# Performance work log

Measured on AMD Instinct MI355X. Metric: run time of the kernel, lower is better.

The kernel has to match this reference:

```python
import jax, jax.numpy as jnp
import numpy as np
import math

B, S, D, H = 2, 2048, 1024, 16
HD = D // H  # head_dims = 64


def setup_inputs() -> dict:
    key = jax.random.key(0)
    ks = jax.random.split(key, 8)
    sc = 1.0 / math.sqrt(D)
    return {
        "queries": jax.random.normal(ks[0], (B, S, D), jnp.float32),
        "keys":    jax.random.normal(ks[1], (B, S, D), jnp.float32),
        "values":  jax.random.normal(ks[2], (B, S, D), jnp.float32),
        # causal mask: 1 where attending allowed, 0 where blocked (masked_fill on ==0)
        "mask": jnp.tril(jnp.ones((S, S), jnp.int32)),
        "Wq": jax.random.normal(ks[3], (D, D), jnp.float32) * sc,
        "bq": jnp.zeros((D,), jnp.float32),
        "Wk": jax.random.normal(ks[4], (D, D), jnp.float32) * sc,
        "bk": jnp.zeros((D,), jnp.float32),
        "Wv": jax.random.normal(ks[5], (D, D), jnp.float32) * sc,
        "bv": jnp.zeros((D,), jnp.float32),
        "Wo": jax.random.normal(ks[6], (D, D), jnp.float32) * sc,
        "bo": jnp.zeros((D,), jnp.float32),
    }


def _split_heads(x):
    # (B, S, D) -> (B, H, S, HD)
    return x.reshape(B, S, H, HD).transpose(0, 2, 1, 3)


def reference(queries, keys, values, mask, Wq, bq, Wk, bk, Wv, bv, Wo, bo):
    q = queries @ Wq + bq
    k = keys @ Wk + bk
    # NOTE: faithful to source quirk — V is projected from the ALREADY-PROJECTED keys
    # (original: keys = self.W_keys(keys); values = self.W_values(keys))
    v = k @ Wv + bv
    q, k, v = _split_heads(q), _split_heads(k), _split_heads(v)
    # naive full NxN attention, as in the source
    scores = jnp.einsum("bhqd,bhkd->bhqk", q, k) / math.sqrt(HD)
    scores = jnp.where(mask == 0, jnp.float32(-1e9), scores)
    probs = jax.nn.softmax(scores, axis=-1)
    attn = jnp.einsum("bhqk,bhkd->bhqd", probs, v)
    attn = attn.transpose(0, 2, 1, 3).reshape(B, S, D)
    return attn @ Wo + bo
```

## Files before the change

kernel.cpp:

```cpp
#include <hip/hip_runtime.h>

typedef unsigned short u16;
typedef unsigned int u32;
typedef __bf16 bf16x8 __attribute__((ext_vector_type(8)));
typedef float f32x4 __attribute__((ext_vector_type(4)));

#define MFMA16(a, b, c) __builtin_amdgcn_mfma_f32_16x16x32_bf16(a, b, c, 0, 0, 0)

__device__ __forceinline__ void gload16(const void* g, void* l) {
  __builtin_amdgcn_global_load_lds((const __attribute__((address_space(1))) void*)g,
                                   (__attribute__((address_space(3))) void*)l, 16, 0, 0);
}

__device__ __forceinline__ u16 f2bf(float f) {
  u32 u = __builtin_bit_cast(u32, f);
  u += 0x7fffu + ((u >> 16) & 1u);
  return (u16)(u >> 16);
}
__device__ __forceinline__ u32 pack2(float a, float b) {
  return (u32)f2bf(a) | ((u32)f2bf(b) << 16);
}

__global__ __launch_bounds__(256) void cvt_kernel(const float* __restrict__ q,
                                                  const float* __restrict__ k,
                                                  u16* __restrict__ qb,
                                                  u16* __restrict__ kb) {
  const float* src = blockIdx.y ? k : q;
  u16* dst = blockIdx.y ? kb : qb;
  size_t i = (size_t)blockIdx.x * 256 + threadIdx.x;
  float4 v = ((const float4*)src)[i];
  ushort4 o;
  o.x = f2bf(v.x); o.y = f2bf(v.y); o.z = f2bf(v.z); o.w = f2bf(v.w);
  ((ushort4*)dst)[i] = o;
}

__global__ __launch_bounds__(256) void wtrans_kernel(const float* W0, const float* W1,
                                                     const float* W2, const float* W3,
                                                     u16* T0, u16* T1, u16* T2, u16* T3) {
  int z = blockIdx.z;
  const float* W = z == 0 ? W0 : z == 1 ? W1 : z == 2 ? W2 : W3;
  u16* T = z == 0 ? T0 : z == 1 ? T1 : z == 2 ? T2 : T3;
  __shared__ float tile[64][65];
  int tr = blockIdx.y * 64, tc = blockIdx.x * 64;
  int tid = threadIdx.x;
  int c4 = (tid & 15) * 4, r0 = tid >> 4;
#pragma unroll
  for (int i = 0; i < 4; i++) {
    int r = r0 + i * 16;
    float4 v = *(const float4*)(W + (size_t)(tr + r) * 1024 + tc + c4);
    tile[r][c4 + 0] = v.x; tile[r][c4 + 1] = v.y;
    tile[r][c4 + 2] = v.z; tile[r][c4 + 3] = v.w;
  }
  __syncthreads();
#pragma unroll
  for (int i = 0; i < 2; i++) {
    int c = tid + i * 256;
    int n = c >> 3, kg = c & 7;
    uint4 o;
    o.x = pack2(tile[kg * 8 + 0][n], tile[kg * 8 + 1][n]);
    o.y = pack2(tile[kg * 8 + 2][n], tile[kg * 8 + 3][n]);
    o.z = pack2(tile[kg * 8 + 4][n], tile[kg * 8 + 5][n]);
    o.w = pack2(tile[kg * 8 + 6][n], tile[kg * 8 + 7][n]);
    *(uint4*)(T + (size_t)(tc + n) * 1024 + tr + kg * 8) = o;
  }
}

template <int MODE>
__global__ __launch_bounds__(256) void gemm_kernel(
    const u16* A0, const u16* B0, const float* bias0, void* C0, float scale0,
    const u16* A1, const u16* B1, const float* bias1, void* C1, float scale1,
    int M, int N, int K) {
  const u16* A = A0; const u16* Bt = B0; const float* bias = bias0; void* Cout = C0;
  float scale = scale0;
  if (blockIdx.z) { A = A1; Bt = B1; bias = bias1; Cout = C1; scale = scale1; }

  __shared__ __attribute__((aligned(16))) char sAB[49152];
  const int tid = threadIdx.x, lane = tid & 63, w = tid >> 6;
  const int l15 = lane & 15, quad = lane >> 4;
  const int wm = (w >> 1) * 64, wn = (w & 1) * 32;
  const int m0 = blockIdx.y * 128, n0 = blockIdx.x * 64;

  const int lrow = lane >> 3, lcg = (lane & 7) ^ lrow;
  const u16* aP[4]; const u16* bP[2];
#pragma unroll
  for (int i = 0; i < 4; i++)
    aP[i] = A + (size_t)(m0 + w * 32 + i * 8 + lrow) * K + lcg * 8;
#pragma unroll
  for (int i = 0; i < 2; i++)
    bP[i] = Bt + (size_t)(n0 + w * 16 + i * 8 + lrow) * K + lcg * 8;

  int aoff[4], boff[2];
#pragma unroll
  for (int t = 0; t < 4; t++) {
    int ra = wm + t * 16 + l15;
    aoff[t] = ra * 128 + ((quad ^ (ra & 7)) * 16);
  }
#pragma unroll
  for (int t = 0; t < 2; t++) {
    int rb = wn + t * 16 + l15;
    boff[t] = 16384 + rb * 128 + ((quad ^ (rb & 7)) * 16);
  }

#pragma unroll
  for (int i = 0; i < 4; i++) { gload16(aP[i], sAB + w * 4096 + i * 1024); aP[i] += 64; }
#pragma unroll
  for (int i = 0; i < 2; i++) { gload16(bP[i], sAB + 16384 + w * 2048 + i * 1024); bP[i] += 64; }

  f32x4 acc[4][2] = {};
  int cur = 0;
  for (int k = 0; k < K; k += 64) {
    __syncthreads();
    if (k + 64 < K) {
      char* dst = sAB + (cur ^ 1) * 24576;
#pragma unroll
      for (int i = 0; i < 4; i++) { gload16(aP[i], dst + w * 4096 + i * 1024); aP[i] += 64; }
#pragma unroll
      for (int i = 0; i < 2; i++) { gload16(bP[i], dst + 16384 + w * 2048 + i * 1024); bP[i] += 64; }
    }
    const char* buf = sAB + cur * 24576;
#pragma unroll
    for (int kt = 0; kt < 2; kt++) {
      bf16x8 af[4], bfr[2];
#pragma unroll
      for (int t = 0; t < 4; t++) af[t] = *(const bf16x8*)(buf + (aoff[t] ^ (kt * 64)));
#pragma unroll
      for (int t = 0; t < 2; t++) bfr[t] = *(const bf16x8*)(buf + (boff[t] ^ (kt * 64)));
#pragma unroll
      for (int mt = 0; mt < 4; mt++)
#pragma unroll
        for (int nt = 0; nt < 2; nt++)
          acc[mt][nt] = MFMA16(af[mt], bfr[nt], acc[mt][nt]);
    }
    cur ^= 1;
  }

#pragma unroll
  for (int nt = 0; nt < 2; nt++) {
    int col = n0 + wn + nt * 16 + l15;
    float bv = bias[col];
#pragma unroll
    for (int mt = 0; mt < 4; mt++) {
      int row = m0 + wm + mt * 16 + quad * 4;
      if (MODE == 0) {
        u16* C = (u16*)Cout;
#pragma unroll
        for (int r = 0; r < 4; r++)
          C[(size_t)(row + r) * N + col] = f2bf((acc[mt][nt][r] + bv) * scale);
      } else if (MODE == 1) {
        u16* C = (u16*)Cout;
        int hh = col >> 6, hd = col & 63;
        int bb = row >> 11, s = row & 2047;
        ushort4 o;
        o.x = f2bf((acc[mt][nt][0] + bv) * scale);
        o.y = f2bf((acc[mt][nt][1] + bv) * scale);
        o.z = f2bf((acc[mt][nt][2] + bv) * scale);
        o.w = f2bf((acc[mt][nt][3] + bv) * scale);
        *(ushort4*)(C + ((size_t)((bb * 16 + hh) * 64 + hd) * 2048 + s)) = o;
      } else {
        float* C = (float*)Cout;
#pragma unroll
        for (int r = 0; r < 4; r++)
          C[(size_t)(row + r) * N + col] = (acc[mt][nt][r] + bv) * scale;
      }
    }
  }
}

__global__ __launch_bounds__(256) void attn_kernel(const u16* __restrict__ qw,
                                                   const u16* __restrict__ kw,
                                                   const u16* __restrict__ vw,
                                                   u16* __restrict__ aout) {
  __shared__ __attribute__((aligned(16))) char sQ[8192];
  __shared__ __attribute__((aligned(16))) char sKV[2][16384];
  __shared__ __attribute__((aligned(16))) char sP[8192];
  const int bh = blockIdx.x, p = blockIdx.y;
  const int b = bh >> 4, h = bh & 15;
  const int tid = threadIdx.x, lane = tid & 63, w = tid >> 6;
  const int l15 = lane & 15, quad = lane >> 4;
  const int lrow = lane >> 3, lcg = (lane & 7) ^ lrow;
  const u16* kb0 = kw + (size_t)(b * 2048) * 1024 + h * 64;
  const u16* vb0 = vw + (size_t)bh * 64 * 2048;

  int qoff[2], poff[2], koff[2][4], voff[2][4], wroff[4];
#pragma unroll
  for (int kt = 0; kt < 2; kt++) {
    int qrow = w * 16 + l15;
    qoff[kt] = qrow * 128 + (((kt * 4 + quad) ^ (qrow & 7)) * 16);
    poff[kt] = w * 2048 + l15 * 128 + (((kt * 4 + quad) ^ (l15 & 7)) * 16);
#pragma unroll
    for (int mt = 0; mt < 4; mt++) {
      int r2 = mt * 16 + l15;
      koff[kt][mt] = r2 * 128 + (((kt * 4 + quad) ^ (r2 & 7)) * 16);
      voff[kt][mt] = 8192 + koff[kt][mt];
    }
  }
#pragma unroll
  for (int mt = 0; mt < 4; mt++)
    wroff[mt] = w * 2048 + l15 * 128 + (((2 * mt + (quad >> 1)) ^ (l15 & 7)) * 16) +
                (quad & 1) * 8;

  for (int phase = 0; phase < 2; ++phase) {
    const int t = phase ? (31 - p) : p;
    __syncthreads();
    {
      const u16* qbase = qw + (size_t)(b * 2048 + t * 64) * 1024 + h * 64;
#pragma unroll
      for (int i = 0; i < 2; i++) {
        int r = w * 16 + i * 8 + lrow;
        gload16(qbase + (size_t)r * 1024 + lcg * 8, sQ + w * 2048 + i * 1024);
        gload16(kb0 + (size_t)r * 1024 + lcg * 8, sKV[0] + w * 2048 + i * 1024);
        gload16(vb0 + (size_t)r * 2048 + lcg * 8, sKV[0] + 8192 + w * 2048 + i * 1024);
      }
    }

    float ls[4] = {0.f, 0.f, 0.f, 0.f};
    f32x4 o[4] = {};
    for (int j = 0; j < t; ++j) {
      __syncthreads();
      {
        char* dstb = sKV[(j + 1) & 1];
#pragma unroll
        for (int i = 0; i < 2; i++) {
          int r = w * 16 + i * 8 + lrow;
          gload16(kb0 + (size_t)((j + 1) * 64 + r) * 1024 + lcg * 8,
                  dstb + w * 2048 + i * 1024);
          gload16(vb0 + (size_t)r * 2048 + (j + 1) * 64 + lcg * 8,
                  dstb + 8192 + w * 2048 + i * 1024);
        }
      }
      const char* bufb = sKV[j & 1];

      f32x4 st[4] = {};
#pragma unroll
      for (int kt = 0; kt < 2; ++kt) {
        bf16x8 qf = *(const bf16x8*)(sQ + qoff[kt]);
        bf16x8 kf[4];
#pragma unroll
        for (int mt = 0; mt < 4; mt++) kf[mt] = *(const bf16x8*)(bufb + koff[kt][mt]);
#pragma unroll
        for (int mt = 0; mt < 4; mt++) st[mt] = MFMA16(kf[mt], qf, st[mt]);
      }
#pragma unroll
      for (int mt = 0; mt < 4; mt++) {
        float e0 = __builtin_amdgcn_exp2f(st[mt][0]);
        float e1 = __builtin_amdgcn_exp2f(st[mt][1]);
        float e2 = __builtin_amdgcn_exp2f(st[mt][2]);
        float e3 = __builtin_amdgcn_exp2f(st[mt][3]);
        ls[mt] += (e0 + e1) + (e2 + e3);
        *(uint2*)(sP + wroff[mt]) = make_uint2(pack2(e0, e1), pack2(e2, e3));
      }
      __asm__ volatile("" ::: "memory");
#pragma unroll
      for (int kt = 0; kt < 2; ++kt) {
        bf16x8 pf = *(const bf16x8*)(sP + poff[kt]);
        bf16x8 vf[4];
#pragma unroll
        for (int mt = 0; mt < 4; mt++) vf[mt] = *(const bf16x8*)(bufb + voff[kt][mt]);
#pragma unroll
        for (int mt = 0; mt < 4; mt++) o[mt] = MFMA16(vf[mt], pf, o[mt]);
      }
    }

    {
      __syncthreads();
      const char* bufb = sKV[t & 1];
      f32x4 st[4] = {};
#pragma unroll
      for (int kt = 0; kt < 2; ++kt) {
        bf16x8 qf = *(const bf16x8*)(sQ + qoff[kt]);
        bf16x8 kf[4];
#pragma unroll
        for (int mt = 0; mt < 4; mt++) kf[mt] = *(const bf16x8*)(bufb + koff[kt][mt]);
#pragma unroll
        for (int mt = 0; mt < 4; mt++) st[mt] = MFMA16(kf[mt], qf, st[mt]);
      }
      const int qcol = w * 16 + l15;
#pragma unroll
      for (int mt = 0; mt < 4; mt++) {
        float e[4];
#pragma unroll
        for (int r = 0; r < 4; r++) {
          float ev = __builtin_amdgcn_exp2f(st[mt][r]);
          if (mt * 16 + quad * 4 + r > qcol) ev = 0.f;
          e[r] = ev;
        }
        ls[mt] += (e[0] + e[1]) + (e[2] + e[3]);
        *(uint2*)(sP + wroff[mt]) = make_uint2(pack2(e[0], e[1]), pack2(e[2], e[3]));
      }
      __asm__ volatile("" ::: "memory");
#pragma unroll
      for (int kt = 0; kt < 2; ++kt) {
        bf16x8 pf = *(const bf16x8*)(sP + poff[kt]);
        bf16x8 vf[4];
#pragma unroll
        for (int mt = 0; mt < 4; mt++) vf[mt] = *(const bf16x8*)(bufb + voff[kt][mt]);
#pragma unroll
        for (int mt = 0; mt < 4; mt++) o[mt] = MFMA16(vf[mt], pf, o[mt]);
      }
    }

    float lsum = (ls[0] + ls[1]) + (ls[2] + ls[3]);
    lsum += __shfl_xor(lsum, 16, 64);
    lsum += __shfl_xor(lsum, 32, 64);
    float inv = 1.0f / lsum;
    int token = b * 2048 + t * 64 + w * 16 + l15;
#pragma unroll
    for (int mt = 0; mt < 4; mt++) {
      int d0 = h * 64 + mt * 16 + quad * 4;
      ushort4 ov;
      ov.x = f2bf(o[mt][0] * inv);
      ov.y = f2bf(o[mt][1] * inv);
      ov.z = f2bf(o[mt][2] * inv);
      ov.w = f2bf(o[mt][3] * inv);
      *(ushort4*)(aout + (size_t)token * 1024 + d0) = ov;
    }
  }
}

extern "C" void kernel_launch(void* const* d_in, const int* in_sizes, int n_in,
                              void* d_out, int out_size, void* d_ws, size_t ws_size,
                              hipStream_t stream) {
  const float* queries = (const float*)d_in[0];
  const float* keys    = (const float*)d_in[1];
  const float* Wq = (const float*)d_in[4];
  const float* bq = (const float*)d_in[5];
  const float* Wk = (const float*)d_in[6];
  const float* bk = (const float*)d_in[7];
  const float* Wv = (const float*)d_in[8];
  const float* bv = (const float*)d_in[9];
  const float* Wo = (const float*)d_in[10];
  const float* bo = (const float*)d_in[11];

  char* ws = (char*)d_ws;
  u16* qb  = (u16*)(ws);
  u16* kb  = (u16*)(ws + (8u << 20));
  u16* qP  = (u16*)(ws + (16u << 20));
  u16* kP  = (u16*)(ws);
  u16* vP  = (u16*)(ws + (8u << 20));
  u16* WqT = (u16*)(ws + (24u << 20));
  u16* WkT = (u16*)(ws + (26u << 20));
  u16* WvT = (u16*)(ws + (28u << 20));
  u16* WoT = (u16*)(ws + (30u << 20));

  const float kscale = 1.4426950408889634f / 8.0f;

  cvt_kernel<<<dim3(4096, 2), 256, 0, stream>>>(queries, keys, qb, kb);
  wtrans_kernel<<<dim3(16, 16, 4), 256, 0, stream>>>(Wq, Wk, Wv, Wo, WqT, WkT, WvT, WoT);
  gemm_kernel<0><<<dim3(16, 32, 2), 256, 0, stream>>>(
      qb, WqT, bq, qP, kscale, kb, WkT, bk, kP, 1.0f, 4096, 1024, 1024);
  gemm_kernel<1><<<dim3(16, 32, 1), 256, 0, stream>>>(
      kP, WvT, bv, vP, 1.0f, kP, WvT, bv, vP, 1.0f, 4096, 1024, 1024);
  attn_kernel<<<dim3(32, 16), 256, 0, stream>>>(qP, kP, vP, qP);
  gemm_kernel<2><<<dim3(16, 32, 1), 256, 0, stream>>>(
      qP, WoT, bo, d_out, 1.0f, qP, WoT, bo, d_out, 1.0f, 4096, 1024, 1024);
}
```

Before: 221.4 us.

## Restructure attention kernel with 32x32 MFMA, split-KV waves, and register-resident P

Rewrites the attention kernel to use 32x32x16 bf16 MFMA tiles. Each pair of waves covers 32 query columns, and the two waves in a pair process alternate KV tiles (split-K) out of a 4-slot LDS ring. Q fragments are held in registers, and P is passed from the QK^T output to the PV input through permlane32_swap instead of an LDS round-trip. Partial outputs are merged across the wave pair through shared memory at the end. The aim is fewer LDS accesses and syncs per tile and better MFMA efficiency. The costs are higher register pressure (launch bounds 256,2), 64KB of LDS, and an extra reduction step.

```diff
diff --git a/kernel.cpp b/kernel.cpp
--- a/kernel.cpp
+++ b/kernel.cpp
@@ -4,8 +4,11 @@
 typedef unsigned int u32;
 typedef __bf16 bf16x8 __attribute__((ext_vector_type(8)));
 typedef float f32x4 __attribute__((ext_vector_type(4)));
+typedef float f32x16 __attribute__((ext_vector_type(16)));
+typedef unsigned int u32x4v __attribute__((ext_vector_type(4)));
 
 #define MFMA16(a, b, c) __builtin_amdgcn_mfma_f32_16x16x32_bf16(a, b, c, 0, 0, 0)
+#define MFMA32(a, b, c) __builtin_amdgcn_mfma_f32_32x32x16_bf16(a, b, c, 0, 0, 0)
 
 __device__ __forceinline__ void gload16(const void* g, void* l) {
   __builtin_amdgcn_global_load_lds((const __attribute__((address_space(1))) void*)g,
@@ -166,153 +169,154 @@
   }
 }
 
-__global__ __launch_bounds__(256) void attn_kernel(const u16* __restrict__ qw,
-                                                   const u16* __restrict__ kw,
-                                                   const u16* __restrict__ vw,
-                                                   u16* __restrict__ aout) {
-  __shared__ __attribute__((aligned(16))) char sQ[8192];
-  __shared__ __attribute__((aligned(16))) char sKV[2][16384];
-  __shared__ __attribute__((aligned(16))) char sP[8192];
+__global__ __launch_bounds__(256, 2) void attn_kernel(const u16* __restrict__ qw,
+                                                      const u16* __restrict__ kw,
+                                                      const u16* __restrict__ vw,
+                                                      u16* __restrict__ aout) {
+  __shared__ __attribute__((aligned(16))) char sKV[4][16384];
   const int bh = blockIdx.x, p = blockIdx.y;
   const int b = bh >> 4, h = bh & 15;
   const int tid = threadIdx.x, lane = tid & 63, w = tid >> 6;
-  const int l15 = lane & 15, quad = lane >> 4;
+  const int g = w & 1, qh = w >> 1;
+  const int c = lane & 31, hi = lane >> 5;
+  const int qcol = qh * 32 + c;
   const int lrow = lane >> 3, lcg = (lane & 7) ^ lrow;
   const u16* kb0 = kw + (size_t)(b * 2048) * 1024 + h * 64;
   const u16* vb0 = vw + (size_t)bh * 64 * 2048;
 
-  int qoff[2], poff[2], koff[2][4], voff[2][4], wroff[4];
-#pragma unroll
-  for (int kt = 0; kt < 2; kt++) {
-    int qrow = w * 16 + l15;
-    qoff[kt] = qrow * 128 + (((kt * 4 + quad) ^ (qrow & 7)) * 16);
-    poff[kt] = w * 2048 + l15 * 128 + (((kt * 4 + quad) ^ (l15 & 7)) * 16);
-#pragma unroll
-    for (int mt = 0; mt < 4; mt++) {
-      int r2 = mt * 16 + l15;
-      koff[kt][mt] = r2 * 128 + (((kt * 4 + quad) ^ (r2 & 7)) * 16);
-      voff[kt][mt] = 8192 + koff[kt][mt];
-    }
-  }
-#pragma unroll
-  for (int mt = 0; mt < 4; mt++)
-    wroff[mt] = w * 2048 + l15 * 128 + (((2 * mt + (quad >> 1)) ^ (l15 & 7)) * 16) +
-                (quad & 1) * 8;
+  int kvoff[2][4];
+#pragma unroll
+  for (int m = 0; m < 2; m++)
+#pragma unroll
+    for (int kt = 0; kt < 4; kt++) {
+      int row = m * 32 + c;
+      kvoff[m][kt] = row * 128 + (((kt * 2 + hi) ^ (row & 7)) * 16);
+    }
+
+  auto stage = [&](int j, int slot) {
+    char* dst = sKV[slot];
+#pragma unroll
+    for (int i = 0; i < 2; i++) {
+      int rr = w * 16 + i * 8 + lrow;
+      gload16(kb0 + (size_t)(j * 64 + rr) * 1024 + lcg * 8, dst + w * 2048 + i * 1024);
+      gload16(vb0 + (size_t)rr * 2048 + j * 64 + lcg * 8, dst + 8192 + w * 2048 + i * 1024);
+    }
+  };
 
   for (int phase = 0; phase < 2; ++phase) {
     const int t = phase ? (31 - p) : p;
     __syncthreads();
+
+    bf16x8 qf[4];
     {
-      const u16* qbase = qw + (size_t)(b * 2048 + t * 64) * 1024 + h * 64;
-#pragma unroll
-      for (int i = 0; i < 2; i++) {
-        int r = w * 16 + i * 8 + lrow;
-        gload16(qbase + (size_t)r * 1024 + lcg * 8, sQ + w * 2048 + i * 1024);
-        gload16(kb0 + (size_t)r * 1024 + lcg * 8, sKV[0] + w * 2048 + i * 1024);
-        gload16(vb0 + (size_t)r * 2048 + lcg * 8, sKV[0] + 8192 + w * 2048 + i * 1024);
-      }
-    }
-
-    float ls[4] = {0.f, 0.f, 0.f, 0.f};
-    f32x4 o[4] = {};
-    for (int j = 0; j < t; ++j) {
+      const u16* qbase =
+          qw + (size_t)(b * 2048 + t * 64 + qcol) * 1024 + h * 64 + hi * 8;
+#pragma unroll
+      for (int kt = 0; kt < 4; kt++) qf[kt] = *(const bf16x8*)(qbase + kt * 16);
+    }
+    stage(0, 0);
+    if (t >= 1) stage(1, 1);
+
+    f32x16 o0 = {}, o1 = {};
+    float lsum = 0.f;
+    const int R = (t + 2) >> 1;
+    for (int r = 0; r < R; ++r) {
       __syncthreads();
-      {
-        char* dstb = sKV[(j + 1) & 1];
-#pragma unroll
-        for (int i = 0; i < 2; i++) {
-          int r = w * 16 + i * 8 + lrow;
-          gload16(kb0 + (size_t)((j + 1) * 64 + r) * 1024 + lcg * 8,
-                  dstb + w * 2048 + i * 1024);
-          gload16(vb0 + (size_t)r * 2048 + (j + 1) * 64 + lcg * 8,
-                  dstb + 8192 + w * 2048 + i * 1024);
+      if (2 * r + 2 <= t) stage(2 * r + 2, (2 * r + 2) & 3);
+      if (2 * r + 3 <= t) stage(2 * r + 3, (2 * r + 3) & 3);
+      const int jg = 2 * r + g;
+      if (jg <= t) {
+        const char* buf = sKV[jg & 3];
+        f32x16 S0 = {}, S1 = {};
+        __builtin_amdgcn_s_setprio(1);
+#pragma unroll
+        for (int kt = 0; kt < 4; kt++) {
+          bf16x8 k0 = *(const bf16x8*)(buf + kvoff[0][kt]);
+          bf16x8 k1 = *(const bf16x8*)(buf + kvoff[1][kt]);
+          S0 = MFMA32(k0, qf[kt], S0);
+          S1 = MFMA32(k1, qf[kt], S1);
         }
-      }
-      const char* bufb = sKV[j & 1];
-
-      f32x4 st[4] = {};
-#pragma unroll
-      for (int kt = 0; kt < 2; ++kt) {
-        bf16x8 qf = *(const bf16x8*)(sQ + qoff[kt]);
-        bf16x8 kf[4];
-#pragma unroll
-        for (int mt = 0; mt < 4; mt++) kf[mt] = *(const bf16x8*)(bufb + koff[kt][mt]);
-#pragma unroll
-        for (int mt = 0; mt < 4; mt++) st[mt] = MFMA16(kf[mt], qf, st[mt]);
-      }
-#pragma unroll
-      for (int mt = 0; mt < 4; mt++) {
-        float e0 = __builtin_amdgcn_exp2f(st[mt][0]);
-        float e1 = __builtin_amdgcn_exp2f(st[mt][1]);
-        float e2 = __builtin_amdgcn_exp2f(st[mt][2]);
-        float e3 = __builtin_amdgcn_exp2f(st[mt][3]);
-        ls[mt] += (e0 + e1) + (e2 + e3);
-        *(uint2*)(sP + wroff[mt]) = make_uint2(pack2(e0, e1), pack2(e2, e3));
-      }
-      __asm__ volatile("" ::: "memory");
-#pragma unroll
-      for (int kt = 0; kt < 2; ++kt) {
-        bf16x8 pf = *(const bf16x8*)(sP + poff[kt]);
-        bf16x8 vf[4];
-#pragma unroll
-        for (int mt = 0; mt < 4; mt++) vf[mt] = *(const bf16x8*)(bufb + voff[kt][mt]);
-#pragma unroll
-        for (int mt = 0; mt < 4; mt++) o[mt] = MFMA16(vf[mt], pf, o[mt]);
-      }
-    }
-
-    {
-      __syncthreads();
-      const char* bufb = sKV[t & 1];
-      f32x4 st[4] = {};
-#pragma unroll
-      for (int kt = 0; kt < 2; ++kt) {
-        bf16x8 qf = *(const bf16x8*)(sQ + qoff[kt]);
-        bf16x8 kf[4];
-#pragma unroll
-        for (int mt = 0; mt < 4; mt++) kf[mt] = *(const bf16x8*)(bufb + koff[kt][mt]);
-#pragma unroll
-        for (int mt = 0; mt < 4; mt++) st[mt] = MFMA16(kf[mt], qf, st[mt]);
-      }
-      const int qcol = w * 16 + l15;
-#pragma unroll
-      for (int mt = 0; mt < 4; mt++) {
-        float e[4];
-#pragma unroll
-        for (int r = 0; r < 4; r++) {
-          float ev = __builtin_amdgcn_exp2f(st[mt][r]);
-          if (mt * 16 + quad * 4 + r > qcol) ev = 0.f;
-          e[r] = ev;
+        __builtin_amdgcn_s_setprio(0);
+        const bool diag = (jg == t);
+        u32 pw0[8], pw1[8];
+        auto epack = [&](const f32x16& S, int mbase, u32* pw) {
+          float e[16];
+#pragma unroll
+          for (int rg = 0; rg < 16; rg++) {
+            float ev = __builtin_amdgcn_exp2f(S[rg]);
+            if (diag) {
+              int row = mbase + (rg & 3) + 8 * (rg >> 2) + 4 * hi;
+              if (row > qcol) ev = 0.f;
+            }
+            e[rg] = ev;
+          }
+          float s = 0.f;
+#pragma unroll
+          for (int rg = 0; rg < 16; rg += 4)
+            s += (e[rg] + e[rg + 1]) + (e[rg + 2] + e[rg + 3]);
+          lsum += s;
+#pragma unroll
+          for (int i = 0; i < 8; i++) pw[i] = pack2(e[2 * i], e[2 * i + 1]);
+        };
+        epack(S0, 0, pw0);
+        epack(S1, 32, pw1);
+        __builtin_amdgcn_s_setprio(1);
+#pragma unroll
+        for (int kt2 = 0; kt2 < 4; kt2++) {
+          const u32* pws = (kt2 < 2) ? pw0 : pw1;
+          const int bb = (kt2 & 1) * 4;
+          auto s0 = __builtin_amdgcn_permlane32_swap(pws[bb + 0], pws[bb + 2], false, false);
+          auto s1 = __builtin_amdgcn_permlane32_swap(pws[bb + 1], pws[bb + 3], false, false);
+          u32x4v pq = {s0[0], s1[0], s0[1], s1[1]};
+          bf16x8 pf = __builtin_bit_cast(bf16x8, pq);
+          bf16x8 v0 = *(const bf16x8*)(buf + 8192 + kvoff[0][kt2]);
+          bf16x8 v1 = *(const bf16x8*)(buf + 8192 + kvoff[1][kt2]);
+          o0 = MFMA32(v0, pf, o0);
+          o1 = MFMA32(v1, pf, o1);
         }
-        ls[mt] += (e[0] + e[1]) + (e[2] + e[3]);
-        *(uint2*)(sP + wroff[mt]) = make_uint2(pack2(e[0], e[1]), pack2(e[2], e[3]));
-      }
-      __asm__ volatile("" ::: "memory");
-#pragma unroll
-      for (int kt = 0; kt < 2; ++kt) {
-        bf16x8 pf = *(const bf16x8*)(sP + poff[kt]);
-        bf16x8 vf[4];
-#pragma unroll
-        for (int mt = 0; mt < 4; mt++) vf[mt] = *(const bf16x8*)(bufb + voff[kt][mt]);
-#pragma unroll
-        for (int mt = 0; mt < 4; mt++) o[mt] = MFMA16(vf[mt], pf, o[mt]);
-      }
-    }
-
-    float lsum = (ls[0] + ls[1]) + (ls[2] + ls[3]);
-    lsum += __shfl_xor(lsum, 16, 64);
-    lsum += __shfl_xor(lsum, 32, 64);
-    float inv = 1.0f / lsum;
-    int token = b * 2048 + t * 64 + w * 16 + l15;
-#pragma unroll
-    for (int mt = 0; mt < 4; mt++) {
-      int d0 = h * 64 + mt * 16 + quad * 4;
-      ushort4 ov;
-      ov.x = f2bf(o[mt][0] * inv);
-      ov.y = f2bf(o[mt][1] * inv);
-      ov.z = f2bf(o[mt][2] * inv);
-      ov.w = f2bf(o[mt][3] * inv);
-      *(ushort4*)(aout + (size_t)token * 1024 + d0) = ov;
+        __builtin_amdgcn_s_setprio(0);
+      }
+    }
+
+    __syncthreads();
+    if (g == 1) {
+      float* red = (float*)(sKV[0] + qh * 8448);
+      float* redl = (float*)(sKV[0] + qh * 8448 + 8192);
+#pragma unroll
+      for (int rg = 0; rg < 16; rg++) {
+        red[lane * 32 + rg] = o0[rg];
+        red[lane * 32 + 16 + rg] = o1[rg];
+      }
+      redl[lane] = lsum;
+    }
+    __syncthreads();
+    if (g == 0) {
+      const float* red = (const float*)(sKV[0] + qh * 8448);
+      const float* redl = (const float*)(sKV[0] + qh * 8448 + 8192);
+#pragma unroll
+      for (int rg = 0; rg < 16; rg++) {
+        o0[rg] += red[lane * 32 + rg];
+        o1[rg] += red[lane * 32 + 16 + rg];
+      }
+      lsum += redl[lane];
+      lsum += __shfl_xor(lsum, 32, 64);
+      float inv = 1.0f / lsum;
+      int token = b * 2048 + t * 64 + qcol;
+      u16* outp = aout + (size_t)token * 1024 + h * 64;
+#pragma unroll
+      for (int i = 0; i < 4; i++) {
+        ushort4 ov;
+        ov.x = f2bf(o0[4 * i + 0] * inv);
+        ov.y = f2bf(o0[4 * i + 1] * inv);
+        ov.z = f2bf(o0[4 * i + 2] * inv);
+        ov.w = f2bf(o0[4 * i + 3] * inv);
+        *(ushort4*)(outp + i * 8 + hi * 4) = ov;
+        ov.x = f2bf(o1[4 * i + 0] * inv);
+        ov.y = f2bf(o1[4 * i + 1] * inv);
+        ov.z = f2bf(o1[4 * i + 2] * inv);
+        ov.w = f2bf(o1[4 * i + 3] * inv);
+        *(ushort4*)(outp + 32 + i * 8 + hi * 4) = ov;
+      }
     }
   }
 }
```

New measurement: 216.1 us. 1.02x faster.
